# Kernel optimization log

Hardware: AMD Instinct MI355X
Metric: run time of the kernel (lower is better)

The kernel has to match this reference:

```python
import jax, jax.numpy as jnp
import numpy as np

GROUPS = 32
EPS = 1e-6


def group_norm(x, gamma, beta):
    B, C, H, W = x.shape
    xg = x.reshape(B, GROUPS, C // GROUPS, H, W)
    mu = xg.mean(axis=(2, 3, 4), keepdims=True)
    var = xg.var(axis=(2, 3, 4), keepdims=True)
    xn = ((xg - mu) / jnp.sqrt(var + EPS)).reshape(B, C, H, W)
    return xn * gamma[None, :, None, None] + beta[None, :, None, None]


def conv1x1(h, w, b):
    # 1x1 conv == channel matmul at every pixel
    return jnp.einsum('bchw,oc->bohw', h, w) + b[None, :, None, None]


def setup_inputs() -> dict:
    key = jax.random.key(0)
    ks = jax.random.split(key, 6)
    B, C, H, W = 2, 512, 64, 64
    s = 1.0 / np.sqrt(C)  # kaiming-ish scale for 1x1 conv weights
    return {
        'x': jax.random.normal(ks[0], (B, C, H, W), jnp.float32),
        'gn_gamma': jnp.ones((C,), jnp.float32),
        'gn_beta': jnp.zeros((C,), jnp.float32),
        'wq': jax.random.normal(ks[1], (C, C), jnp.float32) * s,
        'bq': jnp.zeros((C,), jnp.float32),
        'wk': jax.random.normal(ks[2], (C, C), jnp.float32) * s,
        'bk': jnp.zeros((C,), jnp.float32),
        'wv': jax.random.normal(ks[3], (C, C), jnp.float32) * s,
        'bv': jnp.zeros((C,), jnp.float32),
        'wp': jax.random.normal(ks[4], (C, C), jnp.float32) * s,
        'bp': jnp.zeros((C,), jnp.float32),
    }


def reference(x, gn_gamma, gn_beta, wq, bq, wk, bk, wv, bv, wp, bp):
    h = group_norm(x, gn_gamma, gn_beta)
    q = conv1x1(h, wq, bq)
    k = conv1x1(h, wk, bk)
    v = conv1x1(h, wv, bv)
    B, C, H, W = q.shape
    N = H * W
    qf = q.reshape(B, C, N)
    kf = k.reshape(B, C, N)
    vf = v.reshape(B, C, N)
    # scores[b,i,j] = sum_c q[b,c,i] * k[b,c,j], scaled by 1/sqrt(C)
    scores = jnp.einsum('bci,bcj->bij', qf, kf) * (C ** -0.5)
    attn = jax.nn.softmax(scores, axis=2)  # softmax over keys j
    # out[b,c,i] = sum_j v[b,c,j] * attn[b,i,j]
    out = jnp.einsum('bcj,bij->bci', vf, attn).reshape(B, C, H, W)
    out = conv1x1(out, wp, bp)
    return x + out
```

## Files before the change

kernel.cpp:

```cpp
#include <hip/hip_runtime.h>
#include <hip/hip_bf16.h>
#include <math.h>

#define CDIM 512
#define NPIX 4096
#define BATCH 2
#define NGROUP 32
#define CPG 16
#define EPSV 1e-6f

#define QT 64
#define KT 64

typedef __attribute__((ext_vector_type(4))) float f32x4;
typedef __attribute__((ext_vector_type(8))) short bf16x8;
typedef __attribute__((ext_vector_type(8))) unsigned short ushort8v;
typedef __attribute__((ext_vector_type(4))) unsigned short ushort4v;

__device__ inline unsigned short f2bf(float x) {
  union { __hip_bfloat16 b; unsigned short u; } cv;
  cv.b = __float2bfloat16(x);
  return cv.u;
}
__device__ inline float bf2f(unsigned short u) {
  union { __hip_bfloat16 b; unsigned short u; } cv;
  cv.u = u;
  return __bfloat162float(cv.b);
}

__device__ inline void gload_lds16(const void* g, void* l) {
  __builtin_amdgcn_global_load_lds((const __attribute__((address_space(1))) void*)g,
                                   (__attribute__((address_space(3))) void*)l, 16, 0, 0);
}

__global__ __launch_bounds__(1024)
void gn_kernel(const float* __restrict__ x, const float* __restrict__ gamma,
               const float* __restrict__ beta, float* __restrict__ h) {
  const int NE = CPG * NPIX;
  int b = blockIdx.x >> 5;
  int g = blockIdx.x & 31;
  size_t base = ((size_t)b * CDIM + (size_t)g * CPG) * NPIX;
  const float4* xv = (const float4*)(x + base);
  float4* hv = (float4*)(h + base);
  int t = threadIdx.x;
  float s = 0.f, ss = 0.f;
  for (int i = t; i < NE / 4; i += 1024) {
    float4 v = xv[i];
    s += (v.x + v.y) + (v.z + v.w);
    ss += v.x * v.x + v.y * v.y + v.z * v.z + v.w * v.w;
  }
#pragma unroll
  for (int off = 32; off >= 1; off >>= 1) {
    s += __shfl_down(s, off);
    ss += __shfl_down(ss, off);
  }
  __shared__ float redS[16], redQ[16];
  int wid = t >> 6;
  if ((t & 63) == 0) { redS[wid] = s; redQ[wid] = ss; }
  __syncthreads();
  __shared__ float s_mu, s_rs;
  if (t == 0) {
    float S = 0.f, Q = 0.f;
    for (int w = 0; w < 16; ++w) { S += redS[w]; Q += redQ[w]; }
    float mu = S / NE;
    float var = Q / NE - mu * mu;
    s_mu = mu;
    s_rs = rsqrtf(var + EPSV);
  }
  __syncthreads();
  float mu = s_mu, rs = s_rs;
  for (int i = t; i < NE / 4; i += 1024) {
    int c = g * CPG + (i >> 10);
    float ga = gamma[c] * rs;
    float be = beta[c] - mu * ga;
    float4 v = xv[i];
    v.x = v.x * ga + be;
    v.y = v.y * ga + be;
    v.z = v.z * ga + be;
    v.w = v.w * ga + be;
    hv[i] = v;
  }
}

#define BKc 16
#define WPAD 68

template <int MODE>
__global__ __launch_bounds__(256)
void conv1x1_kernel(const float* __restrict__ W, const float* __restrict__ bias,
                    const float* __restrict__ src, const float* __restrict__ resid,
                    float* __restrict__ dst, unsigned short* __restrict__ dsth,
                    unsigned short* __restrict__ dstl) {
  __shared__ __align__(16) float w_lds[BKc][WPAD];
  __shared__ __align__(16) float h_lds[BKc][64];
  __shared__ __align__(16) unsigned short t_lds[64][72];
  int t = threadIdx.x;
  int nBase = blockIdx.x * 64;
  int oBase = blockIdx.y * 64;
  int b = blockIdx.z;
  const float* srcb = src + (size_t)b * CDIM * NPIX;
  float acc[4][4] = {};
  int o0 = 4 * (t >> 4);
  int j0 = 4 * (t & 15);
  for (int c0 = 0; c0 < CDIM; c0 += BKc) {
    __syncthreads();
#pragma unroll
    for (int kk = 0; kk < 4; ++kk) {
      int idx = t + 256 * kk;
      int o_l = idx >> 4, c_l = idx & 15;
      w_lds[c_l][o_l] = W[(size_t)(oBase + o_l) * CDIM + c0 + c_l];
    }
#pragma unroll
    for (int kk = 0; kk < 4; ++kk) {
      int idx = t + 256 * kk;
      int c_l = idx >> 6, j = idx & 63;
      h_lds[c_l][j] = srcb[(size_t)(c0 + c_l) * NPIX + nBase + j];
    }
    __syncthreads();
#pragma unroll
    for (int kk = 0; kk < BKc; ++kk) {
      float4 a = *(const float4*)&w_lds[kk][o0];
      float4 bv = *(const float4*)&h_lds[kk][j0];
      float av[4] = {a.x, a.y, a.z, a.w};
      float bb[4] = {bv.x, bv.y, bv.z, bv.w};
#pragma unroll
      for (int r = 0; r < 4; ++r)
#pragma unroll
        for (int s2 = 0; s2 < 4; ++s2) acc[r][s2] += av[r] * bb[s2];
    }
  }
  if (MODE == 0) {
#pragma unroll
    for (int r = 0; r < 4; ++r) {
      int o = oBase + o0 + r;
      float bi = bias[o];
      size_t off = ((size_t)b * CDIM + o) * NPIX + nBase + j0;
      float4 out;
      out.x = acc[r][0] + bi;
      out.y = acc[r][1] + bi;
      out.z = acc[r][2] + bi;
      out.w = acc[r][3] + bi;
      float4 rv = *(const float4*)(resid + off);
      out.x += rv.x; out.y += rv.y; out.z += rv.z; out.w += rv.w;
      *(float4*)(dst + off) = out;
    }
  } else if (MODE == 2) {
#pragma unroll
    for (int r = 0; r < 4; ++r) {
      int o = oBase + o0 + r;
      float bi = bias[o];
      size_t off = ((size_t)b * CDIM + o) * NPIX + nBase + j0;
      ushort4v hv, lv;
#pragma unroll
      for (int s2 = 0; s2 < 4; ++s2) {
        float val = acc[r][s2] + bi;
        unsigned short hu = f2bf(val);
        hv[s2] = hu;
        lv[s2] = f2bf(val - bf2f(hu));
      }
      *(ushort4v*)(dsth + off) = hv;
      *(ushort4v*)(dstl + off) = lv;
    }
  } else {
    float biv[4];
#pragma unroll
    for (int r = 0; r < 4; ++r) biv[r] = bias[oBase + o0 + r];
#pragma unroll
    for (int phase = 0; phase < 2; ++phase) {
      __syncthreads();
#pragma unroll
      for (int r = 0; r < 4; ++r)
#pragma unroll
        for (int s2 = 0; s2 < 4; ++s2) {
          float val = acc[r][s2] + biv[r];
          unsigned short hu = f2bf(val);
          t_lds[j0 + s2][o0 + r] = phase == 0 ? hu : f2bf(val - bf2f(hu));
        }
      __syncthreads();
      unsigned short* dp = phase == 0 ? dsth : dstl;
      int row = t >> 2, seg = t & 3;
      size_t goff = ((size_t)b * NPIX + nBase + row) * CDIM + oBase + seg * 16;
#pragma unroll
      for (int e = 0; e < 2; ++e)
        *(ushort8v*)(dp + goff + 8 * e) = *(ushort8v*)&t_lds[row][seg * 16 + 8 * e];
    }
  }
}

template <int KS>
__global__ __launch_bounds__(256, 2)
void attn_kernel(const unsigned short* __restrict__ qt_hi, const unsigned short* __restrict__ qt_lo,
                 const unsigned short* __restrict__ kt_hi, const unsigned short* __restrict__ kt_lo,
                 const unsigned short* __restrict__ v_hi, const unsigned short* __restrict__ v_lo,
                 float* __restrict__ opart, float* __restrict__ mlbuf) {
  const int KEYS_PER = NPIX / KS;
  const int NKT = KEYS_PER / KT;
  __shared__ __align__(16) unsigned short ktile[2][2][64 * 64];
  __shared__ __align__(16) unsigned short plds[64 * 72];
  __shared__ float flds[64];

  int t = threadIdx.x;
  int lane = t & 63;
  int l15 = lane & 15;
  int hh = lane >> 4;
  int w = t >> 6;
  int bid = blockIdx.x;
  int qtile, b, ks;
  if (KS == 4) {
    int g = bid & 7;
    b = g & 1;
    ks = g >> 1;
    qtile = bid >> 3;
  } else {
    qtile = bid & 63;
    b = (bid >> 6) & 1;
    ks = bid >> 7;
  }
  int qBase = qtile * QT;

  const unsigned short* qh = qt_hi + ((size_t)b * NPIX + qBase) * CDIM;
  const unsigned short* ql = qt_lo + ((size_t)b * NPIX + qBase) * CDIM;
  const unsigned short* kh = kt_hi + ((size_t)b * NPIX + ks * KEYS_PER) * CDIM;
  const unsigned short* kl = kt_lo + ((size_t)b * NPIX + ks * KEYS_PER) * CDIM;
  const unsigned short* vh = v_hi + (size_t)b * CDIM * NPIX + ks * KEYS_PER;
  const unsigned short* vl = v_lo + (size_t)b * CDIM * NPIX + ks * KEYS_PER;

  const unsigned short* qrow_h = qh + (size_t)(16 * w + l15) * CDIM + 8 * hh;
  const unsigned short* qrow_l = ql + (size_t)(16 * w + l15) * CDIM + 8 * hh;

  f32x4 Oacc[4][8];
#pragma unroll
  for (int rg = 0; rg < 4; ++rg)
#pragma unroll
    for (int cf = 0; cf < 8; ++cf) Oacc[rg][cf] = (f32x4){0.f, 0.f, 0.f, 0.f};
  float mrow[4], lrow[4];
#pragma unroll
  for (int r = 0; r < 4; ++r) { mrow[r] = -1e30f; lrow[r] = 0.f; }

  const float scale = 0.044194173824159216f;

  auto issue = [&](int ch, int d, int ktof) {
#pragma unroll
    for (int j = 0; j < 4; ++j) {
      int idx = w * 4 + j;
      int hl = idx >> 3;
      int sub = idx & 7;
      const unsigned short* src = hl ? kl : kh;
      int key = sub * 8 + (lane >> 3);
      int cb = (lane & 7) ^ ((lane >> 3) & 7);
      gload_lds16(src + (size_t)(ktof + key) * CDIM + ch * 64 + cb * 8,
                  &ktile[d][hl][sub * 512]);
    }
  };

  issue(0, 0, 0);

  for (int kt = 0; kt < NKT; ++kt) {
    int ktof = kt * KT;
    f32x4 Sacc[4];
#pragma unroll
    for (int f = 0; f < 4; ++f) Sacc[f] = (f32x4){0.f, 0.f, 0.f, 0.f};
    for (int ch = 0; ch < 8; ++ch) {
      int d = ch & 1;
      if (ch < 7) {
        issue(ch + 1, (ch + 1) & 1, ktof);
        asm volatile("s_waitcnt vmcnt(4)" ::: "memory");
      } else {
        asm volatile("s_waitcnt vmcnt(0)" ::: "memory");
      }
      __builtin_amdgcn_s_barrier();
#pragma unroll
      for (int sc = 0; sc < 2; ++sc) {
        int cc = ch * 2 + sc;
        bf16x8 qfh_ = *(const bf16x8*)(qrow_h + 32 * cc);
        bf16x8 qfl_ = *(const bf16x8*)(qrow_l + 32 * cc);
        int cbl = sc * 4 + hh;
#pragma unroll
        for (int f = 0; f < 4; ++f) {
          int key = 16 * f + l15;
          int swz = cbl ^ (key & 7);
          bf16x8 bh = *(const bf16x8*)&ktile[d][0][key * 64 + swz * 8];
          bf16x8 bl = *(const bf16x8*)&ktile[d][1][key * 64 + swz * 8];
          Sacc[f] = __builtin_amdgcn_mfma_f32_16x16x32_bf16(qfh_, bh, Sacc[f], 0, 0, 0);
          Sacc[f] = __builtin_amdgcn_mfma_f32_16x16x32_bf16(qfl_, bh, Sacc[f], 0, 0, 0);
          Sacc[f] = __builtin_amdgcn_mfma_f32_16x16x32_bf16(qfh_, bl, Sacc[f], 0, 0, 0);
        }
      }
      __builtin_amdgcn_s_barrier();
    }
    if (kt + 1 < NKT) issue(0, 0, ktof + KT);
#pragma unroll
    for (int r = 0; r < 4; ++r) {
      float sv[4];
#pragma unroll
      for (int f = 0; f < 4; ++f) sv[f] = Sacc[f][r] * scale;
      float mx = fmaxf(fmaxf(sv[0], sv[1]), fmaxf(sv[2], sv[3]));
#pragma unroll
      for (int off = 1; off <= 8; off <<= 1) mx = fmaxf(mx, __shfl_xor(mx, off));
      float mn = fmaxf(mrow[r], mx);
      float rs = 0.f;
      int prow = 16 * w + 4 * hh + r;
#pragma unroll
      for (int f = 0; f < 4; ++f) {
        float p = __expf(sv[f] - mn);
        rs += p;
        plds[prow * 72 + 16 * f + l15] = f2bf(p);
      }
#pragma unroll
      for (int off = 1; off <= 8; off <<= 1) rs += __shfl_xor(rs, off);
      float fs = __expf(mrow[r] - mn);
      lrow[r] = lrow[r] * fs + rs;
      mrow[r] = mn;
      if (l15 == 0) flds[prow] = fs;
    }
    asm volatile("s_waitcnt lgkmcnt(0)" ::: "memory");
    __builtin_amdgcn_s_barrier();
#pragma unroll
    for (int rg = 0; rg < 4; ++rg) {
      float fr[4];
#pragma unroll
      for (int r = 0; r < 4; ++r) fr[r] = flds[16 * rg + 4 * hh + r];
#pragma unroll
      for (int cf = 0; cf < 8; ++cf)
#pragma unroll
        for (int r = 0; r < 4; ++r) Oacc[rg][cf][r] *= fr[r];
    }
#pragma unroll
    for (int kc = 0; kc < 2; ++kc) {
      bf16x8 ap[4];
#pragma unroll
      for (int rg = 0; rg < 4; ++rg)
        ap[rg] = *(const bf16x8*)&plds[(16 * rg + l15) * 72 + 32 * kc + 8 * hh];
#pragma unroll
      for (int cf = 0; cf < 8; ++cf) {
        int chan = 128 * w + 16 * cf + l15;
        size_t vo = (size_t)chan * NPIX + ktof + 32 * kc + 8 * hh;
        bf16x8 bvh = *(const bf16x8*)(vh + vo);
        bf16x8 bvl = *(const bf16x8*)(vl + vo);
#pragma unroll
        for (int rg = 0; rg < 4; ++rg) {
          Oacc[rg][cf] = __builtin_amdgcn_mfma_f32_16x16x32_bf16(ap[rg], bvh, Oacc[rg][cf], 0, 0, 0);
          Oacc[rg][cf] = __builtin_amdgcn_mfma_f32_16x16x32_bf16(ap[rg], bvl, Oacc[rg][cf], 0, 0, 0);
        }
      }
    }
  }
  size_t obase = (size_t)(b * KS + ks) * NPIX * CDIM;
#pragma unroll
  for (int rg = 0; rg < 4; ++rg)
#pragma unroll
    for (int cf = 0; cf < 8; ++cf) {
      int chan = 128 * w + 16 * cf + l15;
#pragma unroll
      for (int r = 0; r < 4; ++r) {
        int row = 16 * rg + 4 * hh + r;
        opart[obase + (size_t)(qBase + row) * CDIM + chan] = Oacc[rg][cf][r];
      }
    }
  if (l15 == 0) {
    size_t mlb = (size_t)(b * KS + ks) * NPIX;
#pragma unroll
    for (int r = 0; r < 4; ++r) {
      int row = 16 * w + 4 * hh + r;
      mlbuf[(mlb + qBase + row) * 2 + 0] = mrow[r];
      mlbuf[(mlb + qBase + row) * 2 + 1] = lrow[r];
    }
  }
}

template <int KS>
__global__ __launch_bounds__(256)
void combine_kernel(const float* __restrict__ opart, const float* __restrict__ mlbuf,
                    float* __restrict__ ao) {
  __shared__ float tl[64][67];
  __shared__ float wn[KS][64];
  int t = threadIdx.x;
  int r0 = blockIdx.x * 64, c0 = blockIdx.y * 64, b = blockIdx.z;
  if (t < 64) {
    int row = r0 + t;
    float m[KS], l[KS], M = -1e30f;
#pragma unroll
    for (int ks = 0; ks < KS; ++ks) {
      m[ks] = mlbuf[((size_t)(b * KS + ks) * NPIX + row) * 2 + 0];
      l[ks] = mlbuf[((size_t)(b * KS + ks) * NPIX + row) * 2 + 1];
      M = fmaxf(M, m[ks]);
    }
    float den = 0.f;
#pragma unroll
    for (int ks = 0; ks < KS; ++ks) den += __expf(m[ks] - M) * l[ks];
    float rden = 1.f / den;
#pragma unroll
    for (int ks = 0; ks < KS; ++ks) wn[ks][t] = __expf(m[ks] - M) * rden;
  }
  __syncthreads();
  int rr = t >> 4;
  int cc = (t & 15) * 4;
#pragma unroll
  for (int p = 0; p < 4; ++p) {
    int row = rr + 16 * p;
    float ax = 0.f, ay = 0.f, az = 0.f, aw = 0.f;
#pragma unroll
    for (int ks = 0; ks < KS; ++ks) {
      const float* src = opart + ((size_t)(b * KS + ks) * NPIX + r0 + row) * CDIM + c0 + cc;
      float4 v = *(const float4*)src;
      float wv = wn[ks][row];
      ax += wv * v.x; ay += wv * v.y; az += wv * v.z; aw += wv * v.w;
    }
    tl[row][cc + 0] = ax; tl[row][cc + 1] = ay; tl[row][cc + 2] = az; tl[row][cc + 3] = aw;
  }
  __syncthreads();
  int ch2 = t >> 4;
  int rw = (t & 15) * 4;
#pragma unroll
  for (int p = 0; p < 4; ++p) {
    int chn = ch2 + 16 * p;
    float4 o;
    o.x = tl[rw + 0][chn]; o.y = tl[rw + 1][chn]; o.z = tl[rw + 2][chn]; o.w = tl[rw + 3][chn];
    *(float4*)(ao + ((size_t)b * CDIM + c0 + chn) * NPIX + r0 + rw) = o;
  }
}

extern "C" void kernel_launch(void* const* d_in, const int* in_sizes, int n_in,
                              void* d_out, int out_size, void* d_ws, size_t ws_size,
                              hipStream_t stream) {
  const float* x     = (const float*)d_in[0];
  const float* gamma = (const float*)d_in[1];
  const float* beta  = (const float*)d_in[2];
  const float* wq    = (const float*)d_in[3];
  const float* bq    = (const float*)d_in[4];
  const float* wk    = (const float*)d_in[5];
  const float* bk    = (const float*)d_in[6];
  const float* wv    = (const float*)d_in[7];
  const float* bv    = (const float*)d_in[8];
  const float* wp    = (const float*)d_in[9];
  const float* bp    = (const float*)d_in[10];
  float* out = (float*)d_out;

  const size_t per = (size_t)BATCH * CDIM * NPIX;
  size_t need4 = 4 * per * 4 + 6 * per * 2 + (size_t)4 * BATCH * NPIX * 2 * 4;
  const int KS = (ws_size >= need4) ? 4 : 2;

  char* ws = (char*)d_ws;
  float* opart = (float*)ws;
  float* h = (float*)ws;
  unsigned short* qt_hi = (unsigned short*)(ws + (size_t)KS * per * 4);
  unsigned short* qt_lo = qt_hi + per;
  unsigned short* kt_hi = qt_lo + per;
  unsigned short* kt_lo = kt_hi + per;
  unsigned short* v_hi  = kt_lo + per;
  unsigned short* v_lo  = v_hi + per;
  float* mlbuf = (float*)(ws + (size_t)KS * per * 4 + 6 * per * 2);
  float* ao = (float*)qt_hi;

  gn_kernel<<<dim3(BATCH * NGROUP), dim3(1024), 0, stream>>>(x, gamma, beta, h);
  dim3 cgrid(NPIX / 64, CDIM / 64, BATCH);
  conv1x1_kernel<1><<<cgrid, 256, 0, stream>>>(wq, bq, h, nullptr, nullptr, qt_hi, qt_lo);
  conv1x1_kernel<1><<<cgrid, 256, 0, stream>>>(wk, bk, h, nullptr, nullptr, kt_hi, kt_lo);
  conv1x1_kernel<2><<<cgrid, 256, 0, stream>>>(wv, bv, h, nullptr, nullptr, v_hi, v_lo);
  dim3 mgrid(NPIX / 64, CDIM / 64, BATCH);
  if (KS == 4) {
    attn_kernel<4><<<dim3(64 * BATCH * 4), 256, 0, stream>>>(qt_hi, qt_lo, kt_hi, kt_lo,
                                                             v_hi, v_lo, opart, mlbuf);
    combine_kernel<4><<<mgrid, 256, 0, stream>>>(opart, mlbuf, ao);
  } else {
    attn_kernel<2><<<dim3(64 * BATCH * 2), 256, 0, stream>>>(qt_hi, qt_lo, kt_hi, kt_lo,
                                                             v_hi, v_lo, opart, mlbuf);
    combine_kernel<2><<<mgrid, 256, 0, stream>>>(opart, mlbuf, ao);
  }
  conv1x1_kernel<0><<<cgrid, 256, 0, stream>>>(wp, bp, ao, x, out, nullptr, nullptr);
}
```

Before: 763.8 us.

## Switch attention to fp16 split, single-fp16 V, 8-way key split, triple-buffered K

Replaces the bf16 hi/lo split with an fp16 hi/lo split for Q and K. V becomes a single fp16 tensor, which halves the P·V MFMA count and the V traffic. The key split rises to 8, K tiles move to a three-stage buffer with prefetch two windows ahead and one barrier per window, and partial outputs are stored as fp16 in channel-major layout. The combine step becomes a separate weight kernel plus a flat vectorized combine. The cost is lower precision in V and in the partial outputs, a larger workspace, and an extra launch.

```diff
diff --git a/kernel.cpp b/kernel.cpp
--- a/kernel.cpp
+++ b/kernel.cpp
@@ -11,21 +11,22 @@
 
 #define QT 64
 #define KT 64
+#define KS 8
+#define KEYS_PER (NPIX / KS)
+#define NKT (KEYS_PER / KT)
+#define NWIN (NKT * 8)
 
 typedef __attribute__((ext_vector_type(4))) float f32x4;
-typedef __attribute__((ext_vector_type(8))) short bf16x8;
+typedef _Float16 f16x8 __attribute__((ext_vector_type(8)));
 typedef __attribute__((ext_vector_type(8))) unsigned short ushort8v;
 typedef __attribute__((ext_vector_type(4))) unsigned short ushort4v;
 
-__device__ inline unsigned short f2bf(float x) {
-  union { __hip_bfloat16 b; unsigned short u; } cv;
-  cv.b = __float2bfloat16(x);
-  return cv.u;
-}
-__device__ inline float bf2f(unsigned short u) {
-  union { __hip_bfloat16 b; unsigned short u; } cv;
-  cv.u = u;
-  return __bfloat162float(cv.b);
+__device__ inline unsigned short f2h(float x) {
+  _Float16 h = (_Float16)x;
+  return __builtin_bit_cast(unsigned short, h);
+}
+__device__ inline float h2f(unsigned short u) {
+  return (float)__builtin_bit_cast(_Float16, u);
 }
 
 __device__ inline void gload_lds16(const void* g, void* l) {
@@ -150,16 +151,10 @@
       int o = oBase + o0 + r;
       float bi = bias[o];
       size_t off = ((size_t)b * CDIM + o) * NPIX + nBase + j0;
-      ushort4v hv, lv;
-#pragma unroll
-      for (int s2 = 0; s2 < 4; ++s2) {
-        float val = acc[r][s2] + bi;
-        unsigned short hu = f2bf(val);
-        hv[s2] = hu;
-        lv[s2] = f2bf(val - bf2f(hu));
-      }
+      ushort4v hv;
+#pragma unroll
+      for (int s2 = 0; s2 < 4; ++s2) hv[s2] = f2h(acc[r][s2] + bi);
       *(ushort4v*)(dsth + off) = hv;
-      *(ushort4v*)(dstl + off) = lv;
     }
   } else {
     float biv[4];
@@ -173,8 +168,8 @@
 #pragma unroll
         for (int s2 = 0; s2 < 4; ++s2) {
           float val = acc[r][s2] + biv[r];
-          unsigned short hu = f2bf(val);
-          t_lds[j0 + s2][o0 + r] = phase == 0 ? hu : f2bf(val - bf2f(hu));
+          unsigned short hu = f2h(val);
+          t_lds[j0 + s2][o0 + r] = phase == 0 ? hu : f2h(val - h2f(hu));
         }
       __syncthreads();
       unsigned short* dp = phase == 0 ? dsth : dstl;
@@ -187,15 +182,12 @@
   }
 }
 
-template <int KS>
 __global__ __launch_bounds__(256, 2)
 void attn_kernel(const unsigned short* __restrict__ qt_hi, const unsigned short* __restrict__ qt_lo,
                  const unsigned short* __restrict__ kt_hi, const unsigned short* __restrict__ kt_lo,
-                 const unsigned short* __restrict__ v_hi, const unsigned short* __restrict__ v_lo,
-                 float* __restrict__ opart, float* __restrict__ mlbuf) {
-  const int KEYS_PER = NPIX / KS;
-  const int NKT = KEYS_PER / KT;
-  __shared__ __align__(16) unsigned short ktile[2][2][64 * 64];
+                 const unsigned short* __restrict__ vbuf,
+                 unsigned short* __restrict__ opart, float* __restrict__ mlbuf) {
+  __shared__ __align__(16) unsigned short ktile[3][2][64 * 64];
   __shared__ __align__(16) unsigned short plds[64 * 72];
   __shared__ float flds[64];
 
@@ -205,25 +197,17 @@
   int hh = lane >> 4;
   int w = t >> 6;
   int bid = blockIdx.x;
-  int qtile, b, ks;
-  if (KS == 4) {
-    int g = bid & 7;
-    b = g & 1;
-    ks = g >> 1;
-    qtile = bid >> 3;
-  } else {
-    qtile = bid & 63;
-    b = (bid >> 6) & 1;
-    ks = bid >> 7;
-  }
+  int pair = bid & 15;
+  int b = pair >> 3;
+  int ks = pair & 7;
+  int qtile = bid >> 4;
   int qBase = qtile * QT;
 
   const unsigned short* qh = qt_hi + ((size_t)b * NPIX + qBase) * CDIM;
   const unsigned short* ql = qt_lo + ((size_t)b * NPIX + qBase) * CDIM;
   const unsigned short* kh = kt_hi + ((size_t)b * NPIX + ks * KEYS_PER) * CDIM;
   const unsigned short* kl = kt_lo + ((size_t)b * NPIX + ks * KEYS_PER) * CDIM;
-  const unsigned short* vh = v_hi + (size_t)b * CDIM * NPIX + ks * KEYS_PER;
-  const unsigned short* vl = v_lo + (size_t)b * CDIM * NPIX + ks * KEYS_PER;
+  const unsigned short* vb = vbuf + (size_t)b * CDIM * NPIX + ks * KEYS_PER;
 
   const unsigned short* qrow_h = qh + (size_t)(16 * w + l15) * CDIM + 8 * hh;
   const unsigned short* qrow_l = ql + (size_t)(16 * w + l15) * CDIM + 8 * hh;
@@ -239,7 +223,10 @@
 
   const float scale = 0.044194173824159216f;
 
-  auto issue = [&](int ch, int d, int ktof) {
+  auto issue = [&](int g) {
+    int ch = g & 7;
+    int ktof = (g >> 3) * KT;
+    int d = g % 3;
 #pragma unroll
     for (int j = 0; j < 4; ++j) {
       int idx = w * 4 + j;
@@ -253,42 +240,42 @@
     }
   };
 
-  issue(0, 0, 0);
+  issue(0);
+  issue(1);
 
   for (int kt = 0; kt < NKT; ++kt) {
-    int ktof = kt * KT;
     f32x4 Sacc[4];
 #pragma unroll
     for (int f = 0; f < 4; ++f) Sacc[f] = (f32x4){0.f, 0.f, 0.f, 0.f};
     for (int ch = 0; ch < 8; ++ch) {
-      int d = ch & 1;
-      if (ch < 7) {
-        issue(ch + 1, (ch + 1) & 1, ktof);
+      int g = kt * 8 + ch;
+      if (g + 1 < NWIN) {
         asm volatile("s_waitcnt vmcnt(4)" ::: "memory");
       } else {
         asm volatile("s_waitcnt vmcnt(0)" ::: "memory");
       }
       __builtin_amdgcn_s_barrier();
+      if (g + 2 < NWIN) issue(g + 2);
+      int d = g % 3;
 #pragma unroll
       for (int sc = 0; sc < 2; ++sc) {
         int cc = ch * 2 + sc;
-        bf16x8 qfh_ = *(const bf16x8*)(qrow_h + 32 * cc);
-        bf16x8 qfl_ = *(const bf16x8*)(qrow_l + 32 * cc);
+        f16x8 qfh_ = *(const f16x8*)(qrow_h + 32 * cc);
+        f16x8 qfl_ = *(const f16x8*)(qrow_l + 32 * cc);
         int cbl = sc * 4 + hh;
 #pragma unroll
         for (int f = 0; f < 4; ++f) {
           int key = 16 * f + l15;
           int swz = cbl ^ (key & 7);
-          bf16x8 bh = *(const bf16x8*)&ktile[d][0][key * 64 + swz * 8];
-          bf16x8 bl = *(const bf16x8*)&ktile[d][1][key * 64 + swz * 8];
-          Sacc[f] = __builtin_amdgcn_mfma_f32_16x16x32_bf16(qfh_, bh, Sacc[f], 0, 0, 0);
-          Sacc[f] = __builtin_amdgcn_mfma_f32_16x16x32_bf16(qfl_, bh, Sacc[f], 0, 0, 0);
-          Sacc[f] = __builtin_amdgcn_mfma_f32_16x16x32_bf16(qfh_, bl, Sacc[f], 0, 0, 0);
+          f16x8 bh = *(const f16x8*)&ktile[d][0][key * 64 + swz * 8];
+          f16x8 bl = *(const f16x8*)&ktile[d][1][key * 64 + swz * 8];
+          Sacc[f] = __builtin_amdgcn_mfma_f32_16x16x32_f16(qfh_, bh, Sacc[f], 0, 0, 0);
+          Sacc[f] = __builtin_amdgcn_mfma_f32_16x16x32_f16(qfl_, bh, Sacc[f], 0, 0, 0);
+          Sacc[f] = __builtin_amdgcn_mfma_f32_16x16x32_f16(qfh_, bl, Sacc[f], 0, 0, 0);
         }
       }
-      __builtin_amdgcn_s_barrier();
-    }
-    if (kt + 1 < NKT) issue(0, 0, ktof + KT);
+    }
+    int ktof = kt * KT;
 #pragma unroll
     for (int r = 0; r < 4; ++r) {
       float sv[4];
@@ -304,7 +291,7 @@
       for (int f = 0; f < 4; ++f) {
         float p = __expf(sv[f] - mn);
         rs += p;
-        plds[prow * 72 + 16 * f + l15] = f2bf(p);
+        plds[prow * 72 + 16 * f + l15] = f2h(p);
       }
 #pragma unroll
       for (int off = 1; off <= 8; off <<= 1) rs += __shfl_xor(rs, off);
@@ -327,38 +314,33 @@
     }
 #pragma unroll
     for (int kc = 0; kc < 2; ++kc) {
-      bf16x8 ap[4];
+      f16x8 ap[4];
 #pragma unroll
       for (int rg = 0; rg < 4; ++rg)
-        ap[rg] = *(const bf16x8*)&plds[(16 * rg + l15) * 72 + 32 * kc + 8 * hh];
+        ap[rg] = *(const f16x8*)&plds[(16 * rg + l15) * 72 + 32 * kc + 8 * hh];
 #pragma unroll
       for (int cf = 0; cf < 8; ++cf) {
         int chan = 128 * w + 16 * cf + l15;
-        size_t vo = (size_t)chan * NPIX + ktof + 32 * kc + 8 * hh;
-        bf16x8 bvh = *(const bf16x8*)(vh + vo);
-        bf16x8 bvl = *(const bf16x8*)(vl + vo);
-#pragma unroll
-        for (int rg = 0; rg < 4; ++rg) {
-          Oacc[rg][cf] = __builtin_amdgcn_mfma_f32_16x16x32_bf16(ap[rg], bvh, Oacc[rg][cf], 0, 0, 0);
-          Oacc[rg][cf] = __builtin_amdgcn_mfma_f32_16x16x32_bf16(ap[rg], bvl, Oacc[rg][cf], 0, 0, 0);
-        }
+        f16x8 bv = *(const f16x8*)(vb + (size_t)chan * NPIX + ktof + 32 * kc + 8 * hh);
+#pragma unroll
+        for (int rg = 0; rg < 4; ++rg)
+          Oacc[rg][cf] = __builtin_amdgcn_mfma_f32_16x16x32_f16(ap[rg], bv, Oacc[rg][cf], 0, 0, 0);
       }
     }
   }
-  size_t obase = (size_t)(b * KS + ks) * NPIX * CDIM;
+  unsigned short* ob = opart + (size_t)pair * CDIM * NPIX;
 #pragma unroll
   for (int rg = 0; rg < 4; ++rg)
 #pragma unroll
     for (int cf = 0; cf < 8; ++cf) {
       int chan = 128 * w + 16 * cf + l15;
-#pragma unroll
-      for (int r = 0; r < 4; ++r) {
-        int row = 16 * rg + 4 * hh + r;
-        opart[obase + (size_t)(qBase + row) * CDIM + chan] = Oacc[rg][cf][r];
-      }
+      ushort4v pk;
+#pragma unroll
+      for (int r = 0; r < 4; ++r) pk[r] = f2h(Oacc[rg][cf][r]);
+      *(ushort4v*)(ob + (size_t)chan * NPIX + qBase + 16 * rg + 4 * hh) = pk;
     }
   if (l15 == 0) {
-    size_t mlb = (size_t)(b * KS + ks) * NPIX;
+    size_t mlb = (size_t)pair * NPIX;
 #pragma unroll
     for (int r = 0; r < 4; ++r) {
       int row = 16 * w + 4 * hh + r;
@@ -368,56 +350,59 @@
   }
 }
 
-template <int KS>
 __global__ __launch_bounds__(256)
-void combine_kernel(const float* __restrict__ opart, const float* __restrict__ mlbuf,
+void wn_kernel(const float* __restrict__ mlbuf, float* __restrict__ wn) {
+  int idx = blockIdx.x * 256 + threadIdx.x;
+  int b = idx >> 12;
+  int i = idx & (NPIX - 1);
+  float m[KS], l[KS], M = -1e30f;
+#pragma unroll
+  for (int ks = 0; ks < KS; ++ks) {
+    size_t p = ((size_t)(b * KS + ks) * NPIX + i) * 2;
+    m[ks] = mlbuf[p];
+    l[ks] = mlbuf[p + 1];
+    M = fmaxf(M, m[ks]);
+  }
+  float den = 0.f;
+#pragma unroll
+  for (int ks = 0; ks < KS; ++ks) den += __expf(m[ks] - M) * l[ks];
+  float rden = 1.f / den;
+#pragma unroll
+  for (int ks = 0; ks < KS; ++ks)
+    wn[(size_t)(b * KS + ks) * NPIX + i] = __expf(m[ks] - M) * rden;
+}
+
+__global__ __launch_bounds__(256)
+void combine_kernel(const unsigned short* __restrict__ opart, const float* __restrict__ wn,
                     float* __restrict__ ao) {
-  __shared__ float tl[64][67];
-  __shared__ float wn[KS][64];
-  int t = threadIdx.x;
-  int r0 = blockIdx.x * 64, c0 = blockIdx.y * 64, b = blockIdx.z;
-  if (t < 64) {
-    int row = r0 + t;
-    float m[KS], l[KS], M = -1e30f;
-#pragma unroll
-    for (int ks = 0; ks < KS; ++ks) {
-      m[ks] = mlbuf[((size_t)(b * KS + ks) * NPIX + row) * 2 + 0];
-      l[ks] = mlbuf[((size_t)(b * KS + ks) * NPIX + row) * 2 + 1];
-      M = fmaxf(M, m[ks]);
-    }
-    float den = 0.f;
-#pragma unroll
-    for (int ks = 0; ks < KS; ++ks) den += __expf(m[ks] - M) * l[ks];
-    float rden = 1.f / den;
-#pragma unroll
-    for (int ks = 0; ks < KS; ++ks) wn[ks][t] = __expf(m[ks] - M) * rden;
-  }
-  __syncthreads();
-  int rr = t >> 4;
-  int cc = (t & 15) * 4;
-#pragma unroll
-  for (int p = 0; p < 4; ++p) {
-    int row = rr + 16 * p;
-    float ax = 0.f, ay = 0.f, az = 0.f, aw = 0.f;
-#pragma unroll
-    for (int ks = 0; ks < KS; ++ks) {
-      const float* src = opart + ((size_t)(b * KS + ks) * NPIX + r0 + row) * CDIM + c0 + cc;
-      float4 v = *(const float4*)src;
-      float wv = wn[ks][row];
-      ax += wv * v.x; ay += wv * v.y; az += wv * v.z; aw += wv * v.w;
-    }
-    tl[row][cc + 0] = ax; tl[row][cc + 1] = ay; tl[row][cc + 2] = az; tl[row][cc + 3] = aw;
-  }
-  __syncthreads();
-  int ch2 = t >> 4;
-  int rw = (t & 15) * 4;
-#pragma unroll
-  for (int p = 0; p < 4; ++p) {
-    int chn = ch2 + 16 * p;
-    float4 o;
-    o.x = tl[rw + 0][chn]; o.y = tl[rw + 1][chn]; o.z = tl[rw + 2][chn]; o.w = tl[rw + 3][chn];
-    *(float4*)(ao + ((size_t)b * CDIM + c0 + chn) * NPIX + r0 + rw) = o;
-  }
+  size_t idx = (size_t)blockIdx.x * 256 + threadIdx.x;
+  size_t e = idx * 8;
+  int i = (int)(e & (NPIX - 1));
+  size_t bc = e >> 12;
+  int b = (int)(bc >> 9);
+  int c = (int)(bc & 511);
+  float acc[8] = {};
+#pragma unroll
+  for (int ks = 0; ks < KS; ++ks) {
+    const unsigned short* op = opart + ((size_t)(b * KS + ks) * CDIM + c) * NPIX + i;
+    ushort8v ov = *(const ushort8v*)op;
+    const float* wp = wn + (size_t)(b * KS + ks) * NPIX + i;
+    float4 w0 = *(const float4*)wp;
+    float4 w1 = *(const float4*)(wp + 4);
+    acc[0] += w0.x * h2f(ov[0]);
+    acc[1] += w0.y * h2f(ov[1]);
+    acc[2] += w0.z * h2f(ov[2]);
+    acc[3] += w0.w * h2f(ov[3]);
+    acc[4] += w1.x * h2f(ov[4]);
+    acc[5] += w1.y * h2f(ov[5]);
+    acc[6] += w1.z * h2f(ov[6]);
+    acc[7] += w1.w * h2f(ov[7]);
+  }
+  float* dst = ao + bc * NPIX + i;
+  float4 o0 = {acc[0], acc[1], acc[2], acc[3]};
+  float4 o1 = {acc[4], acc[5], acc[6], acc[7]};
+  *(float4*)dst = o0;
+  *(float4*)(dst + 4) = o1;
 }
 
 extern "C" void kernel_launch(void* const* d_in, const int* in_sizes, int n_in,
@@ -437,35 +422,26 @@
   float* out = (float*)d_out;
 
   const size_t per = (size_t)BATCH * CDIM * NPIX;
-  size_t need4 = 4 * per * 4 + 6 * per * 2 + (size_t)4 * BATCH * NPIX * 2 * 4;
-  const int KS = (ws_size >= need4) ? 4 : 2;
-
   char* ws = (char*)d_ws;
-  float* opart = (float*)ws;
+  unsigned short* opart = (unsigned short*)ws;
   float* h = (float*)ws;
-  unsigned short* qt_hi = (unsigned short*)(ws + (size_t)KS * per * 4);
+  unsigned short* qt_hi = (unsigned short*)(ws + (size_t)BATCH * KS * CDIM * NPIX * 2);
   unsigned short* qt_lo = qt_hi + per;
   unsigned short* kt_hi = qt_lo + per;
   unsigned short* kt_lo = kt_hi + per;
-  unsigned short* v_hi  = kt_lo + per;
-  unsigned short* v_lo  = v_hi + per;
-  float* mlbuf = (float*)(ws + (size_t)KS * per * 4 + 6 * per * 2);
-  float* ao = (float*)qt_hi;
+  unsigned short* vbuf  = kt_lo + per;
+  float* mlbuf = (float*)(vbuf + per);
+  float* wn    = mlbuf + (size_t)BATCH * KS * NPIX * 2;
+  float* ao    = (float*)qt_hi;
 
   gn_kernel<<<dim3(BATCH * NGROUP), dim3(1024), 0, stream>>>(x, gamma, beta, h);
   dim3 cgrid(NPIX / 64, CDIM / 64, BATCH);
   conv1x1_kernel<1><<<cgrid, 256, 0, stream>>>(wq, bq, h, nullptr, nullptr, qt_hi, qt_lo);
   conv1x1_kernel<1><<<cgrid, 256, 0, stream>>>(wk, bk, h, nullptr, nullptr, kt_hi, kt_lo);
-  conv1x1_kernel<2><<<cgrid, 256, 0, stream>>>(wv, bv, h, nullptr, nullptr, v_hi, v_lo);
-  dim3 mgrid(NPIX / 64, CDIM / 64, BATCH);
-  if (KS == 4) {
-    attn_kernel<4><<<dim3(64 * BATCH * 4), 256, 0, stream>>>(qt_hi, qt_lo, kt_hi, kt_lo,
-                                                             v_hi, v_lo, opart, mlbuf);
-    combine_kernel<4><<<mgrid, 256, 0, stream>>>(opart, mlbuf, ao);
-  } else {
-    attn_kernel<2><<<dim3(64 * BATCH * 2), 256, 0, stream>>>(qt_hi, qt_lo, kt_hi, kt_lo,
-                                                             v_hi, v_lo, opart, mlbuf);
-    combine_kernel<2><<<mgrid, 256, 0, stream>>>(opart, mlbuf, ao);
-  }
+  conv1x1_kernel<2><<<cgrid, 256, 0, stream>>>(wv, bv, h, nullptr, nullptr, vbuf, nullptr);
+  attn_kernel<<<dim3((NPIX / QT) * BATCH * KS), 256, 0, stream>>>(qt_hi, qt_lo, kt_hi, kt_lo,
+                                                                  vbuf, opart, mlbuf);
+  wn_kernel<<<dim3(BATCH * NPIX / 256), 256, 0, stream>>>(mlbuf, wn);
+  combine_kernel<<<dim3((unsigned)(per / 8 / 256)), 256, 0, stream>>>(opart, wn, ao);
   conv1x1_kernel<0><<<cgrid, 256, 0, stream>>>(wp, bp, ao, x, out, nullptr, nullptr);
 }
```

Result: slower. 797.3 us (+4.4%).
